# Optimization experiments

Measured on AMD Instinct MI355X. Metric: run time of the kernel, lower is better.

## Reference

```python
import jax, jax.numpy as jnp
import numpy as np

B, S = 8, 256
V, D, N, R, H = 32000, 512, 16, 512, 8


def setup_inputs() -> dict:
    key = jax.random.key(0)
    ks = jax.random.split(key, 10)
    sc_e = 0.02
    sc = 1.0 / np.sqrt(D)
    return {
        'x': jax.random.randint(ks[0], (B, S), 0, V),
        'h0': jnp.zeros((N, B, R), jnp.float32),
        'c0': jnp.zeros((N, B, R), jnp.float32),
        'emb': jax.random.normal(ks[1], (V, D), jnp.float32) * sc_e,
        'W_ih': jax.random.normal(ks[2], (N, 4 * R, D), jnp.float32) * sc,
        'b_ih': jnp.zeros((N, 4 * R), jnp.float32),
        'W_hh': jax.random.normal(ks[3], (N, 4 * R, R), jnp.float32) * sc,
        'b_hh': jnp.zeros((N, 4 * R), jnp.float32),
        'W_np': jax.random.normal(ks[4], (N, D, R), jnp.float32) * sc,
        'b_np': jnp.zeros((N, D), jnp.float32),
        'in_w': jax.random.normal(ks[5], (3 * D, D), jnp.float32) * sc,
        'in_b': jnp.zeros((3 * D,), jnp.float32),
        'op_w': jax.random.normal(ks[6], (D, D), jnp.float32) * sc,
        'op_b': jnp.zeros((D,), jnp.float32),
        'ln_g': jnp.ones((D,), jnp.float32),
        'ln_b': jnp.zeros((D,), jnp.float32),
        'head_w': jax.random.normal(ks[7], (V, D), jnp.float32) * sc,
        'head_b': jnp.zeros((V,), jnp.float32),
    }


def _forward(x, h0, c0, emb, W_ih, b_ih, W_hh, b_hh, W_np, b_np,
             in_w, in_b, op_w, op_b, ln_g, ln_b, head_w, head_b):
    b, s = x.shape
    n, g4, d = W_ih.shape
    r = g4 // 4
    h_heads = H
    dh = d // h_heads
    Wq, Wk, Wv = in_w[:d], in_w[d:2 * d], in_w[2 * d:]
    bq, bk, bv = in_b[:d], in_b[d:2 * d], in_b[2 * d:]
    bias = (b_ih + b_hh)[:, None, :]  # (N,1,4R)

    def step(carry, xt):
        h, c = carry  # (N,B,R)
        # batched LSTMCell across neurons (torch gate order i,f,g,o)
        gates = (jnp.einsum('bd,ngd->nbg', xt, W_ih)
                 + jnp.einsum('nbr,ngr->nbg', h, W_hh) + bias)
        i, f, gg, o = jnp.split(gates, 4, axis=-1)
        c_new = jax.nn.sigmoid(f) * c + jax.nn.sigmoid(i) * jnp.tanh(gg)
        h_new = jax.nn.sigmoid(o) * jnp.tanh(c_new)
        nout = jnp.einsum('nbr,ndr->bnd', h_new, W_np) + b_np[None, :, :]  # (B,N,D)
        # mixer multihead attention: query = xt (len 1), key/value = neuron outputs
        q = (xt @ Wq.T + bq).reshape(b, h_heads, dh)
        k = (nout @ Wk.T + bk).reshape(b, n, h_heads, dh)
        v = (nout @ Wv.T + bv).reshape(b, n, h_heads, dh)
        scores = jnp.einsum('bhe,bnhe->bhn', q, k) / np.sqrt(dh).astype(xt.dtype)
        w = jax.nn.softmax(scores, axis=-1)
        att = jnp.einsum('bhn,bnhe->bhe', w, v).reshape(b, d)
        att = att @ op_w.T + op_b
        # residual + LayerNorm
        y = att + xt
        mu = y.mean(-1, keepdims=True)
        var = jnp.mean((y - mu) ** 2, axis=-1, keepdims=True)
        mixed = (y - mu) / jnp.sqrt(var + 1e-5) * ln_g + ln_b
        logit = mixed @ head_w.T + head_b  # (B,V)
        return (h_new, c_new), logit

    xs = emb[x].transpose(1, 0, 2)  # (S,B,D)
    (hf, cf), logits = jax.lax.scan(step, (h0, c0), xs)
    return logits.transpose(1, 0, 2), hf, cf  # (B,S,V), final states


def reference(x, h0, c0, emb, W_ih, b_ih, W_hh, b_hh, W_np, b_np,
              in_w, in_b, op_w, op_b, ln_g, ln_b, head_w, head_b):
    return _forward(x, h0, c0, emb, W_ih, b_ih, W_hh, b_hh, W_np, b_np,
                    in_w, in_b, op_w, op_b, ln_g, ln_b, head_w, head_b)
```

## Files before the change

### kernel.cpp

```cpp
#include <hip/hip_runtime.h>
#include <cstdint>
#include <cstddef>

#define S_ 256
#define B_ 8
#define V_ 32000
#define D_ 512
#define N_ 16
#define R_ 512
#define G4_ 2048
#define SV_ 8192000
#define CHUNK_ 64

typedef __attribute__((ext_vector_type(8))) short short8;
typedef __attribute__((ext_vector_type(4))) float f32x4;
typedef __attribute__((ext_vector_type(4))) unsigned short u16x4;
typedef __attribute__((ext_vector_type(4))) unsigned int u32x4;

__device__ __forceinline__ unsigned short f2b(float f){
  union { float f; unsigned int u; } v; v.f = f;
  unsigned int r = (v.u + 0x7fffu + ((v.u >> 16) & 1u)) >> 16;
  return (unsigned short)r;
}
__device__ __forceinline__ float b2f(unsigned short h){
  union { unsigned int u; float f; } v; v.u = ((unsigned int)h) << 16;
  return v.f;
}

__global__ void k_permute_cast(const float* __restrict__ src, unsigned short* __restrict__ dst,
                               const float* __restrict__ b1, const float* __restrict__ b2,
                               float* __restrict__ bias_out)
{
  int bid = blockIdx.x;
  int n = bid >> 11, g = bid & 2047;
  int q = g >> 9, r = g & 511;
  int gp = (r << 2) | q;
  const float* s = src + (size_t)bid * 512;
  unsigned short* d = dst + ((size_t)(n * 2048 + gp)) * 512;
  int l = threadIdx.x;
  f32x4 a = ((const f32x4*)s)[l*2];
  f32x4 c = ((const f32x4*)s)[l*2+1];
  u16x4 o1, o2;
  o1[0]=f2b(a[0]); o1[1]=f2b(a[1]); o1[2]=f2b(a[2]); o1[3]=f2b(a[3]);
  o2[0]=f2b(c[0]); o2[1]=f2b(c[1]); o2[2]=f2b(c[2]); o2[3]=f2b(c[3]);
  ((u16x4*)d)[l*2] = o1; ((u16x4*)d)[l*2+1] = o2;
  if (l == 0 && bias_out) bias_out[n*2048 + gp] = b1[bid] + b2[bid];
}

__global__ void k_cast(const float* __restrict__ src, unsigned short* __restrict__ dst)
{
  int i = blockIdx.x * 256 + threadIdx.x;
  f32x4 a = ((const f32x4*)src)[i*2];
  f32x4 c = ((const f32x4*)src)[i*2+1];
  u16x4 o1, o2;
  o1[0]=f2b(a[0]); o1[1]=f2b(a[1]); o1[2]=f2b(a[2]); o1[3]=f2b(a[3]);
  o2[0]=f2b(c[0]); o2[1]=f2b(c[1]); o2[2]=f2b(c[2]); o2[3]=f2b(c[3]);
  ((u16x4*)dst)[i*2] = o1; ((u16x4*)dst)[i*2+1] = o2;
}

__global__ void k_transpose_np(const float* __restrict__ src, unsigned short* __restrict__ dst)
{
  __shared__ float tile[64][65];
  int bid = blockIdx.x;
  int n = bid >> 6, dt = (bid >> 3) & 7, rt = bid & 7;
  int tid = threadIdx.x;
  int row = tid >> 2, c4 = (tid & 3) * 16;
  const float* s = src + ((size_t)n*512 + dt*64 + row)*512 + rt*64 + c4;
#pragma unroll
  for (int i = 0; i < 16; i += 4){
    f32x4 v = *(const f32x4*)(s + i);
    tile[row][c4+i] = v[0]; tile[row][c4+i+1] = v[1];
    tile[row][c4+i+2] = v[2]; tile[row][c4+i+3] = v[3];
  }
  __syncthreads();
  unsigned short* d = dst + ((size_t)n*512 + rt*64 + row)*512 + dt*64 + c4;
#pragma unroll
  for (int i = 0; i < 16; i += 4){
    u16x4 o;
    o[0]=f2b(tile[c4+i][row]);   o[1]=f2b(tile[c4+i+1][row]);
    o[2]=f2b(tile[c4+i+2][row]); o[3]=f2b(tile[c4+i+3][row]);
    *(u16x4*)(d + i) = o;
  }
}

__global__ void k_transpose_op(const float* __restrict__ src, float* __restrict__ dst)
{
  __shared__ float tile[64][65];
  int bid = blockIdx.x; int dt = bid >> 3, et = bid & 7;
  int tid = threadIdx.x;
  int row = tid >> 2, c4 = (tid & 3) * 16;
  const float* s = src + ((size_t)(dt*64 + row))*512 + et*64 + c4;
#pragma unroll
  for (int i = 0; i < 16; i += 4){
    f32x4 v = *(const f32x4*)(s + i);
    tile[row][c4+i] = v[0]; tile[row][c4+i+1] = v[1];
    tile[row][c4+i+2] = v[2]; tile[row][c4+i+3] = v[3];
  }
  __syncthreads();
  float* d = dst + ((size_t)(et*64 + row))*512 + dt*64 + c4;
#pragma unroll
  for (int i = 0; i < 16; i++) d[i] = tile[c4+i][row];
}

__global__ void k_embed(const int* __restrict__ x, const float* __restrict__ emb,
                        float* __restrict__ xs, unsigned short* __restrict__ xs_bf)
{
  int row = blockIdx.x;
  int t = row >> 3, b = row & 7;
  int tok = x[b*S_ + t];
  const f32x4* e = (const f32x4*)(emb + (size_t)tok*512);
  int l = threadIdx.x;
  f32x4 v0 = e[l*2], v1 = e[l*2+1];
  f32x4* xo = (f32x4*)(xs + (size_t)row*512);
  xo[l*2] = v0; xo[l*2+1] = v1;
  u16x4 o0, o1;
  o0[0]=f2b(v0[0]); o0[1]=f2b(v0[1]); o0[2]=f2b(v0[2]); o0[3]=f2b(v0[3]);
  o1[0]=f2b(v1[0]); o1[1]=f2b(v1[1]); o1[2]=f2b(v1[2]); o1[3]=f2b(v1[3]);
  u16x4* xb = (u16x4*)(xs_bf + (size_t)row*512);
  xb[l*2] = o0; xb[l*2+1] = o1;
}

__global__ void k_init(const float* __restrict__ h0, const float* __restrict__ c0,
                       float* __restrict__ c_state, unsigned short* __restrict__ h_buf0,
                       unsigned int* __restrict__ flags)
{
  int i = blockIdx.x * 256 + threadIdx.x;
  c_state[i] = c0[i];
  h_buf0[i] = f2b(h0[i]);
  if (blockIdx.x == 0) flags[threadIdx.x] = 0;
}

template<int MODE>
__global__ __launch_bounds__(256)
void k_gemm(const unsigned short* __restrict__ A, const unsigned short* __restrict__ Bm,
            const float* __restrict__ bias, void* __restrict__ Cout,
            int M, int Ncol, int ldc, int nblocks,
            long strideA, long strideB, long strideC, long strideBias)
{
  __shared__ unsigned short lA[128*56];
  __shared__ unsigned short lB[128*56];
  const unsigned short* Ap = A + (size_t)blockIdx.y * strideA;
  const unsigned short* Bp = Bm + (size_t)blockIdx.y * strideB;
  const float* bp = bias ? bias + (size_t)blockIdx.y * strideBias : nullptr;
  int bid = blockIdx.x;
  int mb = bid / nblocks, nb = bid - mb*nblocks;
  int m0 = mb*128, n0 = nb*128;
  int tid = threadIdx.x;
  int wv = tid >> 6, lane = tid & 63;
  int quad = lane >> 4, l16 = lane & 15;
  int wm = wv & 1, wn = wv >> 1;
  f32x4 acc[4][4];
  f32x4 z = {0.f,0.f,0.f,0.f};
#pragma unroll
  for (int i=0;i<4;i++)
#pragma unroll
    for (int j=0;j<4;j++) acc[i][j] = z;

  int lrow = tid >> 2;
  int lkc  = (tid & 3) * 8;
  for (int k0 = 0; k0 < 512; k0 += 32){
    __syncthreads();
#pragma unroll
    for (int h = 0; h < 2; h++){
      int row = lrow + h*64;
      int ar = m0 + row; if (ar >= M) ar = M - 1;
      u32x4 va = *(const u32x4*)(Ap + (size_t)ar*512 + k0 + lkc);
      *(u32x4*)(lA + row*56 + lkc) = va;
      int br = n0 + row; if (br >= Ncol) br = Ncol - 1;
      u32x4 vb = *(const u32x4*)(Bp + (size_t)br*512 + k0 + lkc);
      *(u32x4*)(lB + row*56 + lkc) = vb;
    }
    __syncthreads();
    short8 af[4], bfr[4];
#pragma unroll
    for (int i=0;i<4;i++)
      af[i] = *(const short8*)(lA + (wm*64 + i*16 + l16)*56 + quad*8);
#pragma unroll
    for (int j=0;j<4;j++)
      bfr[j] = *(const short8*)(lB + (wn*64 + j*16 + l16)*56 + quad*8);
#pragma unroll
    for (int i=0;i<4;i++)
#pragma unroll
      for (int j=0;j<4;j++)
        acc[i][j] = __builtin_amdgcn_mfma_f32_16x16x32_bf16(af[i], bfr[j], acc[i][j], 0, 0, 0);
  }
#pragma unroll
  for (int j = 0; j < 4; j++){
    int col = n0 + wn*64 + j*16 + l16;
    float bv = 0.0f;
    if (bp != nullptr && col < Ncol) bv = bp[col];
#pragma unroll
    for (int i = 0; i < 4; i++){
      int rbase = m0 + wm*64 + i*16 + quad*4;
      f32x4 v = acc[i][j];
      if (MODE == 0){
        int tt = rbase >> 3, b0 = rbase & 7;
        int nn = col >> 11, gp = col & 2047;
        u16x4 pk;
        pk[0]=f2b(v[0]+bv); pk[1]=f2b(v[1]+bv); pk[2]=f2b(v[2]+bv); pk[3]=f2b(v[3]+bv);
        *(u16x4*)((unsigned short*)Cout + (((size_t)tt*16 + nn)*2048 + (size_t)gp)*8 + b0) = pk;
      } else if (MODE == 1){
        float* O = (float*)Cout + (size_t)blockIdx.y * strideC;
#pragma unroll
        for (int r = 0; r < 4; r++){
          int m = rbase + r;
          if (m < M && col < Ncol) O[(size_t)m*ldc + col] = v[r] + bv;
        }
      } else if (MODE == 2){
        float* O = (float*)Cout;
#pragma unroll
        for (int r = 0; r < 4; r++){
          int m = rbase + r;
          int bb = m & 7, tt = m >> 3;
          O[(size_t)bb*SV_ + (size_t)tt*V_ + col] = v[r] + bv;
        }
      } else {
        unsigned short* O = (unsigned short*)Cout + (size_t)blockIdx.y * strideC;
#pragma unroll
        for (int r = 0; r < 4; r++){
          int m = rbase + r;
          if (m < M && col < Ncol) O[(size_t)m*ldc + col] = f2b(v[r] + bv);
        }
      }
    }
  }
}

__global__ __launch_bounds__(256, 1)
void k_lstm_persist(const unsigned short* __restrict__ W_hhp,
                    const unsigned short* __restrict__ gates_buf,
                    unsigned short* __restrict__ h_all,
                    unsigned short* __restrict__ h_bufs,
                    float* __restrict__ h_state, float* __restrict__ c_state,
                    unsigned int* __restrict__ flags, int chunk)
{
  __shared__ __align__(16) unsigned char sh[16384];
  __shared__ float gsh[4][2][8][20];
  const int wg = blockIdx.x;
  const int n = wg >> 4, sl = wg & 15;
  const int tid = threadIdx.x;
  const int wv = tid >> 6, lane = tid & 63;
  const int quad = lane >> 4, l16 = lane & 15;
  const int gp0 = sl*128 + wv*32;

  short8 wfr[2][16];
#pragma unroll
  for (int ct = 0; ct < 2; ct++){
    const unsigned short* wp = W_hhp + ((size_t)(n*2048 + gp0 + ct*16 + l16))*512 + quad*8;
#pragma unroll
    for (int k = 0; k < 16; k++)
      wfr[ct][k] = *(const short8*)(wp + k*32);
  }

  const int pb = (lane >> 2) & 7, prl = lane & 3;
  const int rbase = sl*32 + wv*8;
  const int rA = rbase + prl*2;
  float creg[2] = {0.f, 0.f}, hl[2] = {0.f, 0.f};
  if (lane < 32){
    creg[0] = c_state[((size_t)n*8 + pb)*512 + rA];
    creg[1] = c_state[((size_t)n*8 + pb)*512 + rA + 1];
  }

  { u32x4 z = {0,0,0,0};
    *(u32x4*)(sh + 8192 + tid*32) = z;
    *(u32x4*)(sh + 8192 + tid*32 + 16) = z; }

  const int sb = tid >> 5, skc = tid & 31;
  const int sswz = (sb & 7) << 4;
  const int aswz = (l16 & 7) << 4;
  const int fidx = (n << 4) | (lane & 15);

  u16x4 g0, g1;
  if (quad < 2){
    const unsigned short* gptr = gates_buf + ((size_t)n*2048 + gp0 + l16)*8 + quad*4;
    g0 = *(const u16x4*)gptr;
    g1 = *(const u16x4*)(gptr + 128);
  }

  for (int ls = 0; ls < CHUNK_; ls++){
    const int t = chunk*CHUNK_ + ls;
    { const unsigned long long* hin = (const unsigned long long*)
        (h_bufs + (size_t)(t & 1)*65536 + (size_t)n*4096 + (size_t)sb*512 + skc*16);
      unsigned long long q0 = __hip_atomic_load(hin+0, __ATOMIC_RELAXED, __HIP_MEMORY_SCOPE_AGENT);
      unsigned long long q1 = __hip_atomic_load(hin+1, __ATOMIC_RELAXED, __HIP_MEMORY_SCOPE_AGENT);
      unsigned long long q2 = __hip_atomic_load(hin+2, __ATOMIC_RELAXED, __HIP_MEMORY_SCOPE_AGENT);
      unsigned long long q3 = __hip_atomic_load(hin+3, __ATOMIC_RELAXED, __HIP_MEMORY_SCOPE_AGENT);
      union { unsigned long long q[2]; u32x4 v; } a0, a1;
      a0.q[0]=q0; a0.q[1]=q1; a1.q[0]=q2; a1.q[1]=q3;
      *(u32x4*)(sh + sb*1024 + ((skc*32) ^ sswz)) = a0.v;
      *(u32x4*)(sh + sb*1024 + ((skc*32 + 16) ^ sswz)) = a1.v;
    }
    __syncthreads();

    f32x4 acc0, acc1;
    if (quad < 2){
      acc0[0]=b2f(g0[0]); acc0[1]=b2f(g0[1]); acc0[2]=b2f(g0[2]); acc0[3]=b2f(g0[3]);
      acc1[0]=b2f(g1[0]); acc1[1]=b2f(g1[1]); acc1[2]=b2f(g1[2]); acc1[3]=b2f(g1[3]);
    } else {
      f32x4 z = {0.f,0.f,0.f,0.f};
      acc0 = z; acc1 = z;
    }
    if (ls < CHUNK_-1 && quad < 2){
      const unsigned short* gptr = gates_buf + ((size_t)((ls+1)*16 + n)*2048 + gp0 + l16)*8 + quad*4;
      g0 = *(const u16x4*)gptr;
      g1 = *(const u16x4*)(gptr + 128);
    }

#pragma unroll
    for (int k = 0; k < 16; k++){
      short8 af = *(const short8*)(sh + l16*1024 + ((k*64 + quad*16) ^ aswz));
      acc0 = __builtin_amdgcn_mfma_f32_16x16x32_bf16(af, wfr[0][k], acc0, 0, 0, 0);
      acc1 = __builtin_amdgcn_mfma_f32_16x16x32_bf16(af, wfr[1][k], acc1, 0, 0, 0);
    }

    if (quad < 2){
#pragma unroll
      for (int r = 0; r < 4; r++){
        gsh[wv][0][quad*4+r][l16] = acc0[r];
        gsh[wv][1][quad*4+r][l16] = acc1[r];
      }
    }
    __syncthreads();
    if (lane < 32){
      unsigned int hp = 0;
#pragma unroll
      for (int u = 0; u < 2; u++){
        int e = prl*2 + u;
        int ct = e >> 2, sub = e & 3;
        float gi = gsh[wv][ct][pb][sub*4+0];
        float gf = gsh[wv][ct][pb][sub*4+1];
        float gg = gsh[wv][ct][pb][sub*4+2];
        float go = gsh[wv][ct][pb][sub*4+3];
        float cv = creg[u];
        float si = 1.f/(1.f + expf(-gi));
        float sf = 1.f/(1.f + expf(-gf));
        float so = 1.f/(1.f + expf(-go));
        float cn = sf*cv + si*tanhf(gg);
        float hn = so*tanhf(cn);
        creg[u] = cn; hl[u] = hn;
        hp |= ((unsigned int)f2b(hn)) << (u*16);
      }
      unsigned int* hb = (unsigned int*)(h_bufs + (size_t)((t+1)&1)*65536
                                         + ((size_t)n*8 + pb)*512 + rA);
      __hip_atomic_store(hb, hp, __ATOMIC_RELAXED, __HIP_MEMORY_SCOPE_AGENT);
      *(unsigned int*)(h_all + ((size_t)n*2048 + (size_t)t*8 + pb)*512 + rA) = hp;
    }

    if (ls != CHUNK_-1){
      __syncthreads();
      if (tid == 0)
        __hip_atomic_store(flags + wg, (unsigned int)(t+1), __ATOMIC_RELAXED, __HIP_MEMORY_SCOPE_AGENT);
      const unsigned int tgt = (unsigned int)(t+1);
      while (1){
        unsigned int f = __hip_atomic_load(flags + fidx, __ATOMIC_RELAXED, __HIP_MEMORY_SCOPE_AGENT);
        if (__all((int)(f >= tgt))) break;
        __builtin_amdgcn_s_sleep(1);
      }
      asm volatile("" ::: "memory");
    }
  }
  if (lane < 32){
    c_state[((size_t)n*8 + pb)*512 + rA]     = creg[0];
    c_state[((size_t)n*8 + pb)*512 + rA + 1] = creg[1];
    h_state[((size_t)n*8 + pb)*512 + rA]     = hl[0];
    h_state[((size_t)n*8 + pb)*512 + rA + 1] = hl[1];
  }
}

__global__ __launch_bounds__(256)
void k_att2(const float* __restrict__ kv, const float* __restrict__ q_all,
            float* __restrict__ att_all, int c)
{
  __shared__ float sV[16][528];
  __shared__ float sQ[512];
  __shared__ float sS[8][16];
  __shared__ float sW[8][16];
  int row = blockIdx.x, tid = threadIdx.x;
  int grow = c*512 + row;
  for (int idx = tid; idx < 2048; idx += 256){
    int nn = idx >> 7, e4 = (idx & 127) * 4;
    f32x4 v = *(const f32x4*)(kv + ((size_t)nn*512 + row)*1024 + 512 + e4);
    *(f32x4*)&sV[nn][e4] = v;
  }
  if (tid < 128){
    f32x4 q4 = *(const f32x4*)(q_all + (size_t)grow*512 + tid*4);
    *(f32x4*)&sQ[tid*4] = q4;
  }
  __syncthreads();
  if (tid < 128){
    int h = tid >> 4, nn = tid & 15;
    const f32x4* kp = (const f32x4*)(kv + ((size_t)nn*512 + row)*1024 + h*64);
    const f32x4* qp = (const f32x4*)(sQ + h*64);
    float s = 0.f;
#pragma unroll
    for (int i = 0; i < 16; i++){
      f32x4 k4 = kp[i], q4 = qp[i];
      s += k4[0]*q4[0] + k4[1]*q4[1] + k4[2]*q4[2] + k4[3]*q4[3];
    }
    sS[h][nn] = s * 0.125f;
  }
  __syncthreads();
  if (tid < 8){
    float mx = -1e30f;
#pragma unroll
    for (int nn = 0; nn < 16; nn++) mx = fmaxf(mx, sS[tid][nn]);
    float ex[16]; float sum = 0.f;
#pragma unroll
    for (int nn = 0; nn < 16; nn++){ ex[nn] = expf(sS[tid][nn] - mx); sum += ex[nn]; }
    float inv = 1.f/sum;
#pragma unroll
    for (int nn = 0; nn < 16; nn++) sW[tid][nn] = ex[nn]*inv;
  }
  __syncthreads();
  for (int d = tid; d < 512; d += 256){
    int h = d >> 6;
    float a = 0.f;
#pragma unroll
    for (int nn = 0; nn < 16; nn++) a += sW[h][nn] * sV[nn][d];
    att_all[(size_t)grow*512 + d] = a;
  }
}

__global__ __launch_bounds__(256)
void k_opproj(const float* __restrict__ att, const float* __restrict__ opT,
              const float* __restrict__ op_b, const float* __restrict__ xs,
              float* __restrict__ y)
{
  __shared__ float sA[64][36];
  __shared__ float sB[32][68];
  int mb = blockIdx.x >> 3, nb = blockIdx.x & 7;
  int m0 = mb*64, n0 = nb*64;
  int tid = threadIdx.x;
  int ty = tid >> 4, tx = tid & 15;
  float acc[4][4] = {};
  int ra = tid >> 2, ka = (tid & 3) * 8;
  int rb = tid >> 3, cbq = (tid & 7) * 8;
  for (int k0 = 0; k0 < 512; k0 += 32){
    __syncthreads();
    f32x4 a0 = *(const f32x4*)(att + (size_t)(m0+ra)*512 + k0 + ka);
    f32x4 a1 = *(const f32x4*)(att + (size_t)(m0+ra)*512 + k0 + ka + 4);
    f32x4 b0 = *(const f32x4*)(opT + (size_t)(k0+rb)*512 + n0 + cbq);
    f32x4 b1 = *(const f32x4*)(opT + (size_t)(k0+rb)*512 + n0 + cbq + 4);
    *(f32x4*)&sA[ra][ka] = a0;   *(f32x4*)&sA[ra][ka+4] = a1;
    *(f32x4*)&sB[rb][cbq] = b0;  *(f32x4*)&sB[rb][cbq+4] = b1;
    __syncthreads();
#pragma unroll
    for (int kk = 0; kk < 32; kk++){
      float av[4], bv[4];
#pragma unroll
      for (int i=0;i<4;i++) av[i] = sA[ty*4+i][kk];
#pragma unroll
      for (int j=0;j<4;j++) bv[j] = sB[kk][tx*4+j];
#pragma unroll
      for (int i=0;i<4;i++)
#pragma unroll
        for (int j=0;j<4;j++) acc[i][j] += av[i]*bv[j];
    }
  }
  f32x4 ob = *(const f32x4*)(op_b + n0 + tx*4);
#pragma unroll
  for (int i=0;i<4;i++){
    int m = m0 + ty*4 + i;
    f32x4 xr = *(const f32x4*)(xs + (size_t)m*512 + n0 + tx*4);
    f32x4 o;
#pragma unroll
    for (int j=0;j<4;j++) o[j] = acc[i][j] + ob[j] + xr[j];
    *(f32x4*)(y + (size_t)m*512 + n0 + tx*4) = o;
  }
}

__global__ void k_ln(const float* __restrict__ y, const float* __restrict__ ln_g,
                     const float* __restrict__ ln_b, unsigned short* __restrict__ mixed)
{
  int row = blockIdx.x, lane = threadIdx.x;
  const float* yr = y + (size_t)row*512 + lane*8;
  f32x4 v0 = *(const f32x4*)yr;
  f32x4 v1 = *(const f32x4*)(yr + 4);
  float s = v0[0]+v0[1]+v0[2]+v0[3]+v1[0]+v1[1]+v1[2]+v1[3];
#pragma unroll
  for (int off = 32; off; off >>= 1) s += __shfl_xor(s, off);
  float mu = s * (1.f/512.f);
  float d[8];
#pragma unroll
  for (int i=0;i<4;i++){ d[i] = v0[i]-mu; d[4+i] = v1[i]-mu; }
  float p = 0.f;
#pragma unroll
  for (int i=0;i<8;i++) p += d[i]*d[i];
#pragma unroll
  for (int off = 32; off; off >>= 1) p += __shfl_xor(p, off);
  float rstd = rsqrtf(p*(1.f/512.f) + 1e-5f);
  f32x4 g0 = *(const f32x4*)(ln_g + lane*8);
  f32x4 g1 = *(const f32x4*)(ln_g + lane*8 + 4);
  f32x4 b0 = *(const f32x4*)(ln_b + lane*8);
  f32x4 b1 = *(const f32x4*)(ln_b + lane*8 + 4);
  u16x4 o0, o1;
#pragma unroll
  for (int i=0;i<4;i++){
    o0[i] = f2b(d[i]*rstd*g0[i] + b0[i]);
    o1[i] = f2b(d[4+i]*rstd*g1[i] + b1[i]);
  }
  unsigned short* mr = mixed + (size_t)row*512 + lane*8;
  *(u16x4*)mr = o0; *(u16x4*)(mr + 4) = o1;
}

extern "C" void kernel_launch(void* const* d_in, const int* in_sizes, int n_in,
                              void* d_out, int out_size, void* d_ws, size_t ws_size,
                              hipStream_t stream)
{
  const int*   x      = (const int*)  d_in[0];
  const float* h0     = (const float*)d_in[1];
  const float* c0     = (const float*)d_in[2];
  const float* emb    = (const float*)d_in[3];
  const float* W_ih   = (const float*)d_in[4];
  const float* b_ih   = (const float*)d_in[5];
  const float* W_hh   = (const float*)d_in[6];
  const float* b_hh   = (const float*)d_in[7];
  const float* W_np   = (const float*)d_in[8];
  const float* b_np   = (const float*)d_in[9];
  const float* in_w   = (const float*)d_in[10];
  const float* in_b   = (const float*)d_in[11];
  const float* op_w   = (const float*)d_in[12];
  const float* op_b   = (const float*)d_in[13];
  const float* ln_g   = (const float*)d_in[14];
  const float* ln_b   = (const float*)d_in[15];
  const float* head_w = (const float*)d_in[16];
  const float* head_b = (const float*)d_in[17];
  float* out = (float*)d_out;

  char* p = (char*)d_ws;
  unsigned short* gates_buf = (unsigned short*)p;         p += 33554432;
  unsigned short* WnpT      = (unsigned short*)gates_buf;
  unsigned short* W_ihp     = (unsigned short*)p;         p += 33554432;
  unsigned short* W_hhp     = (unsigned short*)p;         p += 33554432;
  unsigned short* headw_bf  = (unsigned short*)p;         p += 32768000;
  unsigned short* A_kv      = (unsigned short*)p;         p += 16777216;
  unsigned short* h_all     = (unsigned short*)p;         p += 33554432;
  float*          xs        = (float*)p;                  p += 4194304;
  float*          q_all     = (float*)p;                  p += 4194304;
  unsigned short* mixed_bf  = (unsigned short*)p;         p += 2097152;
  unsigned short* xs_bf     = (unsigned short*)p;         p += 2097152;
  unsigned short* Wkv_bf    = (unsigned short*)p;         p += 1048576;
  unsigned short* Wq_bf     = (unsigned short*)p;         p += 524288;
  float*          op_wT     = (float*)p;                  p += 1048576;
  float*          h_state   = (float*)p;                  p += 262144;
  float*          c_state   = (float*)p;                  p += 262144;
  unsigned short* h_bufs    = (unsigned short*)p;         p += 262144;
  float*          bias_g    = (float*)p;                  p += 131072;
  float*          bias_kvw  = (float*)p;                  p += 65536;
  unsigned short* bnp_bf    = (unsigned short*)p;         p += 16384;
  unsigned int*   flags     = (unsigned int*)p;           p += 1024;

  k_permute_cast<<<32768, 64, 0, stream>>>(W_ih, W_ihp, b_ih, b_hh, bias_g);
  k_permute_cast<<<32768, 64, 0, stream>>>(W_hh, W_hhp, nullptr, nullptr, nullptr);
  k_cast<<<8000, 256, 0, stream>>>(head_w, headw_bf);
  k_cast<<<256, 256, 0, stream>>>(in_w + 512*512, Wkv_bf);
  k_cast<<<128, 256, 0, stream>>>(in_w, Wq_bf);
  k_cast<<<4, 256, 0, stream>>>(b_np, bnp_bf);
  k_transpose_np<<<1024, 256, 0, stream>>>(W_np, WnpT);
  k_transpose_op<<<64, 256, 0, stream>>>(op_w, op_wT);
  k_gemm<3><<<dim3(32, 16), 256, 0, stream>>>(Wkv_bf, WnpT, nullptr, A_kv,
                                              1024, 512, 512, 4, 0L, 262144L, 524288L, 0L);
  k_gemm<1><<<dim3(8, 1), 256, 0, stream>>>(bnp_bf, Wkv_bf, in_b + 512, bias_kvw,
                                            16, 1024, 1024, 8, 0L, 0L, 0L, 0L);
  k_embed<<<2048, 64, 0, stream>>>(x, emb, xs, xs_bf);
  k_gemm<1><<<dim3(64, 1), 256, 0, stream>>>(xs_bf, Wq_bf, in_b, q_all,
                                             2048, 512, 512, 4, 0L, 0L, 0L, 0L);
  k_init<<<256, 256, 0, stream>>>(h0, c0, c_state, h_bufs, flags);

  for (int c = 0; c < 4; c++){
    k_gemm<0><<<dim3(1024, 1), 256, 0, stream>>>(xs_bf + (size_t)c*262144, W_ihp, bias_g,
                                                 gates_buf, 512, 32768, 0, 256, 0L, 0L, 0L, 0L);
    k_lstm_persist<<<256, 256, 0, stream>>>(W_hhp, gates_buf, h_all, h_bufs,
                                            h_state, c_state, flags, c);
  }

  float* kv_chunk = (float*)gates_buf;
  float* att_all  = (float*)W_ihp;
  float* y_all    = att_all + 2048*512;
  for (int c = 0; c < 4; c++){
    k_gemm<1><<<dim3(32, 16), 256, 0, stream>>>(h_all + (size_t)c*262144, A_kv, bias_kvw,
                                                kv_chunk, 512, 1024, 1024, 8,
                                                1048576L, 524288L, 524288L, 1024L);
    k_att2<<<512, 256, 0, stream>>>(kv_chunk, q_all, att_all, c);
  }
  k_opproj<<<256, 256, 0, stream>>>(att_all, op_wT, op_b, xs, y_all);
  k_ln<<<2048, 64, 0, stream>>>(y_all, ln_g, ln_b, mixed_bf);

  k_gemm<2><<<dim3(4000, 1), 256, 0, stream>>>(mixed_bf, headw_bf, head_b, out,
                                               2048, 32000, 0, 250, 0L, 0L, 0L, 0L);
  hipMemcpyAsync(out + (size_t)B_*SV_,         h_state, 65536*sizeof(float),
                 hipMemcpyDeviceToDevice, stream);
  hipMemcpyAsync(out + (size_t)B_*SV_ + 65536, c_state, 65536*sizeof(float),
                 hipMemcpyDeviceToDevice, stream);
}
```

Before: 1.814 ms.

## Use per-wave flags and double-buffered LDS to cut barriers in persistent LSTM

Replaces the per-workgroup flag and its two trailing barriers with per-wavefront flags, 64 per neuron. Each wave publishes its own h slice and then spins on all 64 flags of its neuron at the start of the next step. The h staging buffer in LDS is double-buffered so the barrier after the gate write can be dropped. The MFMA chain is split into two accumulators for more instruction-level parallelism, and the gates prefetch is moved to after the publish. The change enlarges the flag array and drops the s_sleep in the spin loop, which risks more contention on the flag cache lines. The gsh reads after removing the barrier rely on each wave touching only its own rows.

```diff
diff --git a/kernel.cpp b/kernel.cpp
--- a/kernel.cpp
+++ b/kernel.cpp
@@ -127,7 +127,7 @@
   int i = blockIdx.x * 256 + threadIdx.x;
   c_state[i] = c0[i];
   h_buf0[i] = f2b(h0[i]);
-  if (blockIdx.x == 0) flags[threadIdx.x] = 0;
+  if (blockIdx.x < 4) flags[blockIdx.x * 256 + threadIdx.x] = 0;
 }
 
 template<int MODE>
@@ -234,7 +234,7 @@
                     float* __restrict__ h_state, float* __restrict__ c_state,
                     unsigned int* __restrict__ flags, int chunk)
 {
-  __shared__ __align__(16) unsigned char sh[16384];
+  __shared__ __align__(16) unsigned char sh[2][16384];
   __shared__ float gsh[4][2][8][20];
   const int wg = blockIdx.x;
   const int n = wg >> 4, sl = wg & 15;
@@ -262,13 +262,14 @@
   }
 
   { u32x4 z = {0,0,0,0};
-    *(u32x4*)(sh + 8192 + tid*32) = z;
-    *(u32x4*)(sh + 8192 + tid*32 + 16) = z; }
+    *(u32x4*)(&sh[0][8192] + tid*32) = z;
+    *(u32x4*)(&sh[0][8192] + tid*32 + 16) = z;
+    *(u32x4*)(&sh[1][8192] + tid*32) = z;
+    *(u32x4*)(&sh[1][8192] + tid*32 + 16) = z; }
 
   const int sb = tid >> 5, skc = tid & 31;
   const int sswz = (sb & 7) << 4;
   const int aswz = (l16 & 7) << 4;
-  const int fidx = (n << 4) | (lane & 15);
 
   u16x4 g0, g1;
   if (quad < 2){
@@ -279,6 +280,18 @@
 
   for (int ls = 0; ls < CHUNK_; ls++){
     const int t = chunk*CHUNK_ + ls;
+
+    {
+      const unsigned int tgt = (unsigned int)t;
+      while (1){
+        unsigned int f = __hip_atomic_load(flags + (n << 6) + lane,
+                                           __ATOMIC_RELAXED, __HIP_MEMORY_SCOPE_AGENT);
+        if (__all((int)(f >= tgt))) break;
+      }
+      asm volatile("" ::: "memory");
+    }
+
+    unsigned char* shb = sh[t & 1];
     { const unsigned long long* hin = (const unsigned long long*)
         (h_bufs + (size_t)(t & 1)*65536 + (size_t)n*4096 + (size_t)sb*512 + skc*16);
       unsigned long long q0 = __hip_atomic_load(hin+0, __ATOMIC_RELAXED, __HIP_MEMORY_SCOPE_AGENT);
@@ -287,31 +300,30 @@
       unsigned long long q3 = __hip_atomic_load(hin+3, __ATOMIC_RELAXED, __HIP_MEMORY_SCOPE_AGENT);
       union { unsigned long long q[2]; u32x4 v; } a0, a1;
       a0.q[0]=q0; a0.q[1]=q1; a1.q[0]=q2; a1.q[1]=q3;
-      *(u32x4*)(sh + sb*1024 + ((skc*32) ^ sswz)) = a0.v;
-      *(u32x4*)(sh + sb*1024 + ((skc*32 + 16) ^ sswz)) = a1.v;
+      *(u32x4*)(shb + sb*1024 + ((skc*32) ^ sswz)) = a0.v;
+      *(u32x4*)(shb + sb*1024 + ((skc*32 + 16) ^ sswz)) = a1.v;
     }
     __syncthreads();
 
-    f32x4 acc0, acc1;
-    if (quad < 2){
-      acc0[0]=b2f(g0[0]); acc0[1]=b2f(g0[1]); acc0[2]=b2f(g0[2]); acc0[3]=b2f(g0[3]);
-      acc1[0]=b2f(g1[0]); acc1[1]=b2f(g1[1]); acc1[2]=b2f(g1[2]); acc1[3]=b2f(g1[3]);
-    } else {
-      f32x4 z = {0.f,0.f,0.f,0.f};
-      acc0 = z; acc1 = z;
-    }
-    if (ls < CHUNK_-1 && quad < 2){
-      const unsigned short* gptr = gates_buf + ((size_t)((ls+1)*16 + n)*2048 + gp0 + l16)*8 + quad*4;
-      g0 = *(const u16x4*)gptr;
-      g1 = *(const u16x4*)(gptr + 128);
-    }
-
-#pragma unroll
-    for (int k = 0; k < 16; k++){
-      short8 af = *(const short8*)(sh + l16*1024 + ((k*64 + quad*16) ^ aswz));
-      acc0 = __builtin_amdgcn_mfma_f32_16x16x32_bf16(af, wfr[0][k], acc0, 0, 0, 0);
-      acc1 = __builtin_amdgcn_mfma_f32_16x16x32_bf16(af, wfr[1][k], acc1, 0, 0, 0);
-    }
+    f32x4 acc0, acc1, acc0b, acc1b;
+    { f32x4 z = {0.f,0.f,0.f,0.f}; acc0b = z; acc1b = z;
+      if (quad < 2){
+        acc0[0]=b2f(g0[0]); acc0[1]=b2f(g0[1]); acc0[2]=b2f(g0[2]); acc0[3]=b2f(g0[3]);
+        acc1[0]=b2f(g1[0]); acc1[1]=b2f(g1[1]); acc1[2]=b2f(g1[2]); acc1[3]=b2f(g1[3]);
+      } else { acc0 = z; acc1 = z; }
+    }
+
+#pragma unroll
+    for (int k = 0; k < 8; k++){
+      short8 afA = *(const short8*)(shb + l16*1024 + (((2*k)*64   + quad*16) ^ aswz));
+      short8 afB = *(const short8*)(shb + l16*1024 + (((2*k+1)*64 + quad*16) ^ aswz));
+      acc0  = __builtin_amdgcn_mfma_f32_16x16x32_bf16(afA, wfr[0][2*k],   acc0,  0, 0, 0);
+      acc1  = __builtin_amdgcn_mfma_f32_16x16x32_bf16(afA, wfr[1][2*k],   acc1,  0, 0, 0);
+      acc0b = __builtin_amdgcn_mfma_f32_16x16x32_bf16(afB, wfr[0][2*k+1], acc0b, 0, 0, 0);
+      acc1b = __builtin_amdgcn_mfma_f32_16x16x32_bf16(afB, wfr[1][2*k+1], acc1b, 0, 0, 0);
+    }
+    acc0 = acc0 + acc0b;
+    acc1 = acc1 + acc1b;
 
     if (quad < 2){
 #pragma unroll
@@ -320,9 +332,8 @@
         gsh[wv][1][quad*4+r][l16] = acc1[r];
       }
     }
-    __syncthreads();
+    unsigned int hp = 0;
     if (lane < 32){
-      unsigned int hp = 0;
 #pragma unroll
       for (int u = 0; u < 2; u++){
         int e = prl*2 + u;
@@ -343,20 +354,19 @@
       unsigned int* hb = (unsigned int*)(h_bufs + (size_t)((t+1)&1)*65536
                                          + ((size_t)n*8 + pb)*512 + rA);
       __hip_atomic_store(hb, hp, __ATOMIC_RELAXED, __HIP_MEMORY_SCOPE_AGENT);
+    }
+
+    asm volatile("s_waitcnt vmcnt(0)" ::: "memory");
+    if (lane == 0)
+      __hip_atomic_store(flags + (n << 6) + (sl << 2) + wv, (unsigned int)(t+1),
+                         __ATOMIC_RELAXED, __HIP_MEMORY_SCOPE_AGENT);
+
+    if (lane < 32)
       *(unsigned int*)(h_all + ((size_t)n*2048 + (size_t)t*8 + pb)*512 + rA) = hp;
-    }
-
-    if (ls != CHUNK_-1){
-      __syncthreads();
-      if (tid == 0)
-        __hip_atomic_store(flags + wg, (unsigned int)(t+1), __ATOMIC_RELAXED, __HIP_MEMORY_SCOPE_AGENT);
-      const unsigned int tgt = (unsigned int)(t+1);
-      while (1){
-        unsigned int f = __hip_atomic_load(flags + fidx, __ATOMIC_RELAXED, __HIP_MEMORY_SCOPE_AGENT);
-        if (__all((int)(f >= tgt))) break;
-        __builtin_amdgcn_s_sleep(1);
-      }
-      asm volatile("" ::: "memory");
+    if (ls < CHUNK_-1 && quad < 2){
+      const unsigned short* gptr = gates_buf + ((size_t)((ls+1)*16 + n)*2048 + gp0 + l16)*8 + quad*4;
+      g0 = *(const u16x4*)gptr;
+      g1 = *(const u16x4*)(gptr + 128);
     }
   }
   if (lane < 32){
@@ -548,7 +558,7 @@
   float*          bias_g    = (float*)p;                  p += 131072;
   float*          bias_kvw  = (float*)p;                  p += 65536;
   unsigned short* bnp_bf    = (unsigned short*)p;         p += 16384;
-  unsigned int*   flags     = (unsigned int*)p;           p += 1024;
+  unsigned int*   flags     = (unsigned int*)p;           p += 4096;
 
   k_permute_cast<<<32768, 64, 0, stream>>>(W_ih, W_ihp, b_ih, b_hh, bias_g);
   k_permute_cast<<<32768, 64, 0, stream>>>(W_hh, W_hhp, nullptr, nullptr, nullptr);
```

Result: slower. 2.015 ms (+11.1%).
